# Kernel tuning notes

Hardware: AMD Instinct MI355X
Metric: run time of the kernel (lower is better)

## Reference

```python
import jax, jax.numpy as jnp
import numpy as np

H = 16          # num_attention_heads
D = 64          # attention_head_size
BUCKET = 128    # bucket_size
MAX_BUCKETS = 32
TEMP = 0.75
SINKHORN_ITERS = 5
NOISE_KEY = 42  # fixed key for gumbel routing noise (deterministic reference)


def _sinkhorn_route(pl, W, key):
    # pl: [b,h,buckets,d] bucket summaries, W: [h,d,buckets]
    R = jnp.einsum('bhid,hdf->bhif', pl, W)  # [b,h,buckets,buckets]
    u = jax.random.uniform(key, R.shape, R.dtype)
    gumbel = -jnp.log(-jnp.log(u + 1e-6) + 1e-6)
    R = (R + gumbel) / TEMP
    for _ in range(SINKHORN_ITERS):
        R = R - jax.scipy.special.logsumexp(R, axis=-1, keepdims=True)
        R = R - jax.scipy.special.logsumexp(R, axis=-2, keepdims=True)
    return jnp.exp(R)


def setup_inputs() -> dict:
    key = jax.random.key(0)
    kq, kk, kv, kwk, kwv = jax.random.split(key, 5)
    q = jax.random.normal(kq, (64, 4096, 64), jnp.float32)
    k = jax.random.normal(kk, (64, 4096, 64), jnp.float32)
    v = jax.random.normal(kv, (64, 4096, 64), jnp.float32)
    W_keys = jax.random.normal(kwk, (H, D, MAX_BUCKETS), jnp.float32)
    W_vals = jax.random.normal(kwv, (H, D, MAX_BUCKETS), jnp.float32)
    return {'q': q, 'k': k, 'v': v, 'W_keys': W_keys, 'W_vals': W_vals}


def reference(q, q_unused=None, *, _=None, **__):
    raise RuntimeError  # placeholder, replaced below


def reference(q, k, v, W_keys, W_vals):
    t, d = q.shape[1], q.shape[2]
    buckets = t // BUCKET
    # [b, h, buckets, bucket_size, d]
    b_q = q.reshape(-1, H, buckets, BUCKET, d)
    b_k = k.reshape(-1, H, buckets, BUCKET, d)
    b_v = v.reshape(-1, H, buckets, BUCKET, d)

    pl_k = b_k.sum(axis=-2)  # [b,h,buckets,d]
    R_k = _sinkhorn_route(pl_k, W_keys[..., :buckets], jax.random.key(NOISE_KEY))
    # NOTE: original also computes R_v / b_v_r but never uses them for output.

    b_k = jnp.einsum('bhij,bhjsd->bhisd', R_k, b_k) + b_k

    dots = jnp.einsum('bhuid,bhujd->bhuij', b_q, b_k) * (d ** -0.5)
    probs = jax.nn.softmax(dots, axis=-1)
    out = jnp.einsum('bhuij,bhujd->bhuid', probs, b_v)  # [b,h,buckets,s,d]
    return out.reshape(-1, t, d)
```

## Files before the change

### kernel.cpp

```cpp
#include <hip/hip_runtime.h>
#include <math.h>

#define BH 64
#define NB 32
#define BS 128
#define DHEAD 64

typedef __attribute__((ext_vector_type(8))) short bf16x8;
typedef __attribute__((ext_vector_type(4))) float f32x4;

#define LDVT 128
#define LDP 136


__device__ __forceinline__ unsigned rotl32(unsigned x, int d) {
    return (x << d) | (x >> (32 - d));
}

__device__ __forceinline__ void threefry2x32(unsigned k0, unsigned k1,
                                             unsigned& x0, unsigned& x1) {
    const unsigned ks0 = k0, ks1 = k1, ks2 = k0 ^ k1 ^ 0x1BD11BDAu;
    const int r0[4] = {13, 15, 26, 6};
    const int r1[4] = {17, 29, 16, 24};
    x0 += ks0; x1 += ks1;
    #pragma unroll
    for (int i = 0; i < 4; i++) { x0 += x1; x1 = rotl32(x1, r0[i]); x1 ^= x0; }
    x0 += ks1; x1 += ks2 + 1u;
    #pragma unroll
    for (int i = 0; i < 4; i++) { x0 += x1; x1 = rotl32(x1, r1[i]); x1 ^= x0; }
    x0 += ks2; x1 += ks0 + 2u;
    #pragma unroll
    for (int i = 0; i < 4; i++) { x0 += x1; x1 = rotl32(x1, r0[i]); x1 ^= x0; }
    x0 += ks0; x1 += ks1 + 3u;
    #pragma unroll
    for (int i = 0; i < 4; i++) { x0 += x1; x1 = rotl32(x1, r1[i]); x1 ^= x0; }
    x0 += ks1; x1 += ks2 + 4u;
    #pragma unroll
    for (int i = 0; i < 4; i++) { x0 += x1; x1 = rotl32(x1, r0[i]); x1 ^= x0; }
    x0 += ks2; x1 += ks0 + 5u;
}

__device__ __forceinline__ float jax_uniform_part(unsigned f) {
    unsigned x0 = 0u, x1 = f;
    threefry2x32(0u, 42u, x0, x1);
    unsigned bits = x0 ^ x1;
    return __uint_as_float((bits >> 9) | 0x3F800000u) - 1.0f;
}

__global__ void __launch_bounds__(256)
pl_kernel(const float* __restrict__ k, float* __restrict__ pl) {
    int blk = blockIdx.x;
    int tid = threadIdx.x;
    int w = tid >> 6, l = tid & 63;
    int rcls = l >> 4, c4 = l & 15;
    const float4* base = (const float4*)(k + (size_t)blk * 8192);

    float4 acc = {0.f, 0.f, 0.f, 0.f};
    #pragma unroll
    for (int t = 0; t < 8; t++) {
        float4 x = base[(w * 32 + t * 4 + rcls) * 16 + c4];
        acc.x += x.x; acc.y += x.y; acc.z += x.z; acc.w += x.w;
    }
    #pragma unroll
    for (int off = 16; off < 64; off <<= 1) {
        acc.x += __shfl_xor(acc.x, off);
        acc.y += __shfl_xor(acc.y, off);
        acc.z += __shfl_xor(acc.z, off);
        acc.w += __shfl_xor(acc.w, off);
    }
    __shared__ float4 red[4][16];
    if (rcls == 0) red[w][c4] = acc;
    __syncthreads();
    if (tid < 64) {
        int g = tid >> 2, j = tid & 3;
        float s = ((const float*)&red[0][g])[j] + ((const float*)&red[1][g])[j]
                + ((const float*)&red[2][g])[j] + ((const float*)&red[3][g])[j];
        pl[blk * 64 + tid] = s;
    }
}

__global__ void route_kernel(const float* __restrict__ pl, const float* __restrict__ Wk,
                             float* __restrict__ Rout) {
    int bh = blockIdx.x;
    int h = bh & 15;
    int tid = threadIdx.x;
    int i = tid >> 5, j = tid & 31;

    __shared__ float plS[NB * DHEAD];
    __shared__ float T[32 * 33];
    __shared__ float colL[32];

    for (int x = tid; x < NB * DHEAD; x += 1024) plS[x] = pl[bh * NB * DHEAD + x];
    __syncthreads();

    float acc = 0.f;
    #pragma unroll 8
    for (int d2 = 0; d2 < DHEAD; d2++)
        acc += plS[i * DHEAD + d2] * Wk[(h * DHEAD + d2) * NB + j];

    unsigned f = (unsigned)bh * 1024u + (unsigned)i * 32u + (unsigned)j;
    float u = jax_uniform_part(f);
    float g = -__logf(-__logf(u + 1e-6f) + 1e-6f);
    float val = (acc + g) / 0.75f;

    for (int it = 0; it < 5; it++) {
        float m = val;
        #pragma unroll
        for (int off = 1; off < 32; off <<= 1) m = fmaxf(m, __shfl_xor(m, off, 32));
        float s = __expf(val - m);
        #pragma unroll
        for (int off = 1; off < 32; off <<= 1) s += __shfl_xor(s, off, 32);
        val -= m + __logf(s);

        T[i * 33 + j] = val;
        __syncthreads();
        float tv = T[j * 33 + i];
        float m2 = tv;
        #pragma unroll
        for (int off = 1; off < 32; off <<= 1) m2 = fmaxf(m2, __shfl_xor(m2, off, 32));
        float s2 = __expf(tv - m2);
        #pragma unroll
        for (int off = 1; off < 32; off <<= 1) s2 += __shfl_xor(s2, off, 32);
        if (j == 0) colL[i] = m2 + __logf(s2);
        __syncthreads();
        val -= colL[j];
    }
    Rout[bh * 1024 + i * 32 + j] = __expf(val) + (i == j ? 1.0f : 0.0f);
}

__global__ void __launch_bounds__(256)
mix_kernel(const float* __restrict__ k, const float* __restrict__ Rp,
           unsigned short* __restrict__ khl) {
    __shared__ float X[32][260];
    int bh = blockIdx.x >> 5;
    int tile = blockIdx.x & 31;
    const size_t kbase = (size_t)bh * 262144;
    const int col0 = tile * 256;

    {
        int j = threadIdx.x >> 3;
        int cs = (threadIdx.x & 7) * 32;
        const float4* src = (const float4*)(k + kbase + (size_t)j * 8192 + col0 + cs);
        #pragma unroll
        for (int t = 0; t < 8; t++)
            *((float4*)&X[j][cs + 4 * t]) = src[t];
    }
    __syncthreads();

    const int col = threadIdx.x;
    float xv[32];
    #pragma unroll
    for (int j = 0; j < 32; j++) xv[j] = X[j][col];

    const float* Rb = Rp + bh * 1024;
    const int slot = col0 + col;
    const int s = slot >> 6, d = slot & 63;
    const int idx = s * 64 + (d ^ ((s & 7) << 3));
    const bool even = (col & 1) == 0;

    #pragma unroll 4
    for (int i = 0; i < 32; i++) {
        float acc = 0.f;
        #pragma unroll
        for (int j = 0; j < 32; j++) acc = fmaf(Rb[i * 32 + j], xv[j], acc);
        unsigned kb = __float_as_uint(acc);
        unsigned hiu = kb >> 16;
        float rem = acc - __uint_as_float(kb & 0xFFFF0000u);
        unsigned lou = __float_as_uint(rem) >> 16;
        unsigned oh = (unsigned)__shfl_xor((int)hiu, 1);
        unsigned ol = (unsigned)__shfl_xor((int)lou, 1);
        if (even) {
            unsigned short* bp = khl + ((size_t)(bh * 32 + i) << 14);
            *(unsigned*)&bp[idx]        = hiu | (oh << 16);
            *(unsigned*)&bp[idx + 8192] = lou | (ol << 16);
        }
    }
}

__global__ void __launch_bounds__(256)
attn_mfma_kernel(const float* __restrict__ q, const unsigned short* __restrict__ khl,
                 const float* __restrict__ v, float* __restrict__ out) {
    __shared__ __align__(16) unsigned short smem[8192 + 17408];
    unsigned short* VtS = smem;
    unsigned short* KhS = smem + 8192;
    unsigned short* KlS = smem + 16384;
    unsigned short* PbS = smem + 8192;

    const int tid = threadIdx.x;
    const int w = tid >> 6, lane = tid & 63;
    const int quad = lane >> 4, l15 = lane & 15;
    const int row0 = 32 * w;
    const size_t base = (size_t)blockIdx.x * (BS * DHEAD);

    {
        const char* src = (const char*)(khl + ((size_t)blockIdx.x << 14)) + tid * 16;
        char* dst = (char*)KhS + tid * 16;
        #pragma unroll
        for (int c = 0; c < 8; c++)
            __builtin_amdgcn_global_load_lds(
                (const __attribute__((address_space(1))) unsigned int*)(src + c * 4096),
                (__attribute__((address_space(3))) unsigned int*)(dst + c * 4096),
                16, 0, 0);
    }

    {
        int rp = tid >> 2;
        int c0 = (tid & 3) * 16;
        const float* v0 = v + base + (size_t)(2 * rp) * DHEAD + c0;
        const float* v1 = v0 + DHEAD;
        #pragma unroll
        for (int x = 0; x < 4; x++) {
            float4 a = ((const float4*)v0)[x];
            float4 b = ((const float4*)v1)[x];
            float fa[4] = {a.x, a.y, a.z, a.w};
            float fb[4] = {b.x, b.y, b.z, b.w};
            #pragma unroll
            for (int y = 0; y < 4; y++) {
                int c = c0 + 4 * x + y;
                unsigned lo = (__float_as_uint(fa[y]) + 0x8000u) >> 16;
                unsigned hi = (__float_as_uint(fb[y]) + 0x8000u) >> 16;
                unsigned swz = ((unsigned)((c ^ (c >> 4)) & 15)) << 3;
                unsigned idx = (unsigned)c * LDVT + (((unsigned)(2 * rp)) ^ swz);
                *(unsigned*)&VtS[idx] = lo | (hi << 16);
            }
        }
    }

    bf16x8 qh[2][2], ql[2][2];
    #pragma unroll
    for (int ti = 0; ti < 2; ti++) {
        #pragma unroll
        for (int kk = 0; kk < 2; kk++) {
            const float* qp = q + base + (size_t)(row0 + 16 * ti + l15) * DHEAD
                              + kk * 32 + quad * 8;
            float4 a = ((const float4*)qp)[0];
            float4 b = ((const float4*)qp)[1];
            float f[8] = {a.x, a.y, a.z, a.w, b.x, b.y, b.z, b.w};
            #pragma unroll
            for (int j = 0; j < 8; j++) {
                float qs = f[j] * 0.125f;
                unsigned bits = __float_as_uint(qs);
                unsigned short hi = (unsigned short)(bits >> 16);
                float rem = qs - __uint_as_float(bits & 0xFFFF0000u);
                unsigned short lo = (unsigned short)(__float_as_uint(rem) >> 16);
                qh[ti][kk][j] = (short)hi;
                ql[ti][kk][j] = (short)lo;
            }
        }
    }
    __syncthreads();

    f32x4 acc[2][8];
    #pragma unroll
    for (int ti = 0; ti < 2; ti++)
        #pragma unroll
        for (int tc = 0; tc < 8; tc++)
            acc[ti][tc] = (f32x4){0.f, 0.f, 0.f, 0.f};

    #pragma unroll
    for (int tc = 0; tc < 8; tc++) {
        const int jrow = 16 * tc + l15;
        const int swzk = (jrow & 7) << 3;
        const int rbase = jrow * 64;
        bf16x8 bh0 = *(const bf16x8*)&KhS[rbase + ((quad * 8 + 0)  ^ swzk)];
        bf16x8 bh1 = *(const bf16x8*)&KhS[rbase + ((quad * 8 + 32) ^ swzk)];
        bf16x8 bl0 = *(const bf16x8*)&KlS[rbase + ((quad * 8 + 0)  ^ swzk)];
        bf16x8 bl1 = *(const bf16x8*)&KlS[rbase + ((quad * 8 + 32) ^ swzk)];
        __builtin_amdgcn_s_setprio(1);
        #pragma unroll
        for (int ti = 0; ti < 2; ti++) {
            f32x4 c = acc[ti][tc];
            c = __builtin_amdgcn_mfma_f32_16x16x32_bf16(qh[ti][0], bh0, c, 0, 0, 0);
            c = __builtin_amdgcn_mfma_f32_16x16x32_bf16(qh[ti][1], bh1, c, 0, 0, 0);
            c = __builtin_amdgcn_mfma_f32_16x16x32_bf16(ql[ti][0], bh0, c, 0, 0, 0);
            c = __builtin_amdgcn_mfma_f32_16x16x32_bf16(ql[ti][1], bh1, c, 0, 0, 0);
            c = __builtin_amdgcn_mfma_f32_16x16x32_bf16(qh[ti][0], bl0, c, 0, 0, 0);
            c = __builtin_amdgcn_mfma_f32_16x16x32_bf16(qh[ti][1], bl1, c, 0, 0, 0);
            acc[ti][tc] = c;
        }
        __builtin_amdgcn_s_setprio(0);
    }

    float mrow[2][4], lrow[2][4];
    #pragma unroll
    for (int ti = 0; ti < 2; ti++)
        #pragma unroll
        for (int r = 0; r < 4; r++) {
            float m = acc[ti][0][r];
            #pragma unroll
            for (int tc = 1; tc < 8; tc++) m = fmaxf(m, acc[ti][tc][r]);
            #pragma unroll
            for (int off = 1; off < 16; off <<= 1)
                m = fmaxf(m, __shfl_xor(m, off, 64));
            mrow[ti][r] = m;
        }
    #pragma unroll
    for (int ti = 0; ti < 2; ti++)
        #pragma unroll
        for (int r = 0; r < 4; r++) {
            float s = 0.f;
            #pragma unroll
            for (int tc = 0; tc < 8; tc++) {
                float p = __expf(acc[ti][tc][r] - mrow[ti][r]);
                acc[ti][tc][r] = p;
                s += p;
            }
            #pragma unroll
            for (int off = 1; off < 16; off <<= 1)
                s += __shfl_xor(s, off, 64);
            lrow[ti][r] = s;
        }

    __syncthreads();

    #pragma unroll
    for (int ti = 0; ti < 2; ti++)
        #pragma unroll
        for (int tc = 0; tc < 8; tc++)
            #pragma unroll
            for (int r = 0; r < 4; r++) {
                int prow = row0 + 16 * ti + quad * 4 + r;
                unsigned pb = __float_as_uint(acc[ti][tc][r]);
                PbS[prow * LDP + 16 * tc + l15] = (unsigned short)((pb + 0x8000u) >> 16);
            }
    __syncthreads();

    f32x4 oacc[2][4];
    #pragma unroll
    for (int ti = 0; ti < 2; ti++)
        #pragma unroll
        for (int tc = 0; tc < 4; tc++)
            oacc[ti][tc] = (f32x4){0.f, 0.f, 0.f, 0.f};

    #pragma unroll
    for (int kc = 0; kc < 4; kc++) {
        bf16x8 aP[2];
        #pragma unroll
        for (int ti = 0; ti < 2; ti++)
            aP[ti] = *(const bf16x8*)&PbS[(row0 + 16 * ti + l15) * LDP + kc * 32 + quad * 8];
        __builtin_amdgcn_s_setprio(1);
        #pragma unroll
        for (int tc = 0; tc < 4; tc++) {
            unsigned n = (unsigned)(16 * tc + l15);
            unsigned swz = ((n ^ (n >> 4)) & 15u) << 3;
            unsigned idx = n * LDVT + (((unsigned)(kc * 32 + quad * 8)) ^ swz);
            bf16x8 vb = *(const bf16x8*)&VtS[idx];
            #pragma unroll
            for (int ti = 0; ti < 2; ti++)
                oacc[ti][tc] = __builtin_amdgcn_mfma_f32_16x16x32_bf16(aP[ti], vb, oacc[ti][tc], 0, 0, 0);
        }
        __builtin_amdgcn_s_setprio(0);
    }

    float inv[2][4];
    #pragma unroll
    for (int ti = 0; ti < 2; ti++)
        #pragma unroll
        for (int r = 0; r < 4; r++) inv[ti][r] = 1.0f / lrow[ti][r];

    #pragma unroll
    for (int ti = 0; ti < 2; ti++)
        #pragma unroll
        for (int tc = 0; tc < 4; tc++)
            #pragma unroll
            for (int r = 0; r < 4; r++) {
                int orow = row0 + 16 * ti + quad * 4 + r;
                out[base + (size_t)orow * DHEAD + 16 * tc + l15] = oacc[ti][tc][r] * inv[ti][r];
            }
}

extern "C" void kernel_launch(void* const* d_in, const int* in_sizes, int n_in,
                              void* d_out, int out_size, void* d_ws, size_t ws_size,
                              hipStream_t stream) {
    const float* q  = (const float*)d_in[0];
    const float* k  = (const float*)d_in[1];
    const float* v  = (const float*)d_in[2];
    const float* Wk = (const float*)d_in[3];
    float* out = (float*)d_out;

    unsigned short* khl = (unsigned short*)d_ws;
    float* pl = (float*)(khl + (size_t)33554432);
    float* R  = pl + (size_t)131072;

    pl_kernel<<<dim3(BH * NB), dim3(256), 0, stream>>>(k, pl);
    route_kernel<<<dim3(BH), dim3(1024), 0, stream>>>(pl, Wk, R);
    mix_kernel<<<dim3(BH * NB), dim3(256), 0, stream>>>(k, R, khl);
    attn_mfma_kernel<<<dim3(BH * NB), dim3(256), 0, stream>>>(q, khl, v, out);
}
```

Before: 276.3 us.

## Keep softmax probabilities in registers via bpermute and shrink LDS footprint

The QK^T MFMA operands are swapped so each lane holds a full query row's scores, which allows row max/sum reductions with just two cross-quad shuffles. Probabilities are normalized and packed to bf16 in registers, then redistributed into the PV A-operand layout with ds_bpermute instead of a round trip through a padded LDS buffer. V is held in registers until K is consumed so V^T can reuse K's LDS space, cutting shared memory from about 50KB to 32KB, and launch bounds ask for 4 blocks per SM. This trades extra register pressure and permute instructions for higher occupancy and less LDS traffic.

```diff
diff --git a/kernel.cpp b/kernel.cpp
--- a/kernel.cpp
+++ b/kernel.cpp
@@ -10,7 +10,6 @@
 typedef __attribute__((ext_vector_type(4))) float f32x4;
 
 #define LDVT 128
-#define LDP 136
 
 
 __device__ __forceinline__ unsigned rotl32(unsigned x, int d) {
@@ -45,6 +44,10 @@
     threefry2x32(0u, 42u, x0, x1);
     unsigned bits = x0 ^ x1;
     return __uint_as_float((bits >> 9) | 0x3F800000u) - 1.0f;
+}
+
+__device__ __forceinline__ unsigned rn16(float x) {
+    return (__float_as_uint(x) + 0x8000u) >> 16;
 }
 
 __global__ void __launch_bounds__(256)
@@ -177,14 +180,13 @@
     }
 }
 
-__global__ void __launch_bounds__(256)
+__global__ void __launch_bounds__(256, 4)
 attn_mfma_kernel(const float* __restrict__ q, const unsigned short* __restrict__ khl,
                  const float* __restrict__ v, float* __restrict__ out) {
-    __shared__ __align__(16) unsigned short smem[8192 + 17408];
+    __shared__ __align__(16) unsigned short smem[16384];
+    unsigned short* KhS = smem;
+    unsigned short* KlS = smem + 8192;
     unsigned short* VtS = smem;
-    unsigned short* KhS = smem + 8192;
-    unsigned short* KlS = smem + 16384;
-    unsigned short* PbS = smem + 8192;
 
     const int tid = threadIdx.x;
     const int w = tid >> 6, lane = tid & 63;
@@ -203,10 +205,11 @@
                 16, 0, 0);
     }
 
+    const int rp = tid >> 2;
+    const int c0v = (tid & 3) * 16;
+    unsigned vt[16];
     {
-        int rp = tid >> 2;
-        int c0 = (tid & 3) * 16;
-        const float* v0 = v + base + (size_t)(2 * rp) * DHEAD + c0;
+        const float* v0 = v + base + (size_t)(2 * rp) * DHEAD + c0v;
         const float* v1 = v0 + DHEAD;
         #pragma unroll
         for (int x = 0; x < 4; x++) {
@@ -215,14 +218,8 @@
             float fa[4] = {a.x, a.y, a.z, a.w};
             float fb[4] = {b.x, b.y, b.z, b.w};
             #pragma unroll
-            for (int y = 0; y < 4; y++) {
-                int c = c0 + 4 * x + y;
-                unsigned lo = (__float_as_uint(fa[y]) + 0x8000u) >> 16;
-                unsigned hi = (__float_as_uint(fb[y]) + 0x8000u) >> 16;
-                unsigned swz = ((unsigned)((c ^ (c >> 4)) & 15)) << 3;
-                unsigned idx = (unsigned)c * LDVT + (((unsigned)(2 * rp)) ^ swz);
-                *(unsigned*)&VtS[idx] = lo | (hi << 16);
-            }
+            for (int y = 0; y < 4; y++)
+                vt[4 * x + y] = rn16(fa[y]) | (rn16(fb[y]) << 16);
         }
     }
 
@@ -262,67 +259,68 @@
         const int jrow = 16 * tc + l15;
         const int swzk = (jrow & 7) << 3;
         const int rbase = jrow * 64;
-        bf16x8 bh0 = *(const bf16x8*)&KhS[rbase + ((quad * 8 + 0)  ^ swzk)];
-        bf16x8 bh1 = *(const bf16x8*)&KhS[rbase + ((quad * 8 + 32) ^ swzk)];
-        bf16x8 bl0 = *(const bf16x8*)&KlS[rbase + ((quad * 8 + 0)  ^ swzk)];
-        bf16x8 bl1 = *(const bf16x8*)&KlS[rbase + ((quad * 8 + 32) ^ swzk)];
+        bf16x8 kh0 = *(const bf16x8*)&KhS[rbase + ((quad * 8 + 0)  ^ swzk)];
+        bf16x8 kh1 = *(const bf16x8*)&KhS[rbase + ((quad * 8 + 32) ^ swzk)];
+        bf16x8 kl0 = *(const bf16x8*)&KlS[rbase + ((quad * 8 + 0)  ^ swzk)];
+        bf16x8 kl1 = *(const bf16x8*)&KlS[rbase + ((quad * 8 + 32) ^ swzk)];
         __builtin_amdgcn_s_setprio(1);
         #pragma unroll
         for (int ti = 0; ti < 2; ti++) {
             f32x4 c = acc[ti][tc];
-            c = __builtin_amdgcn_mfma_f32_16x16x32_bf16(qh[ti][0], bh0, c, 0, 0, 0);
-            c = __builtin_amdgcn_mfma_f32_16x16x32_bf16(qh[ti][1], bh1, c, 0, 0, 0);
-            c = __builtin_amdgcn_mfma_f32_16x16x32_bf16(ql[ti][0], bh0, c, 0, 0, 0);
-            c = __builtin_amdgcn_mfma_f32_16x16x32_bf16(ql[ti][1], bh1, c, 0, 0, 0);
-            c = __builtin_amdgcn_mfma_f32_16x16x32_bf16(qh[ti][0], bl0, c, 0, 0, 0);
-            c = __builtin_amdgcn_mfma_f32_16x16x32_bf16(qh[ti][1], bl1, c, 0, 0, 0);
+            c = __builtin_amdgcn_mfma_f32_16x16x32_bf16(kh0, qh[ti][0], c, 0, 0, 0);
+            c = __builtin_amdgcn_mfma_f32_16x16x32_bf16(kh1, qh[ti][1], c, 0, 0, 0);
+            c = __builtin_amdgcn_mfma_f32_16x16x32_bf16(kh0, ql[ti][0], c, 0, 0, 0);
+            c = __builtin_amdgcn_mfma_f32_16x16x32_bf16(kh1, ql[ti][1], c, 0, 0, 0);
+            c = __builtin_amdgcn_mfma_f32_16x16x32_bf16(kl0, qh[ti][0], c, 0, 0, 0);
+            c = __builtin_amdgcn_mfma_f32_16x16x32_bf16(kl1, qh[ti][1], c, 0, 0, 0);
             acc[ti][tc] = c;
         }
         __builtin_amdgcn_s_setprio(0);
     }
 
-    float mrow[2][4], lrow[2][4];
-    #pragma unroll
-    for (int ti = 0; ti < 2; ti++)
-        #pragma unroll
-        for (int r = 0; r < 4; r++) {
-            float m = acc[ti][0][r];
-            #pragma unroll
-            for (int tc = 1; tc < 8; tc++) m = fmaxf(m, acc[ti][tc][r]);
-            #pragma unroll
-            for (int off = 1; off < 16; off <<= 1)
-                m = fmaxf(m, __shfl_xor(m, off, 64));
-            mrow[ti][r] = m;
-        }
-    #pragma unroll
-    for (int ti = 0; ti < 2; ti++)
-        #pragma unroll
-        for (int r = 0; r < 4; r++) {
-            float s = 0.f;
-            #pragma unroll
-            for (int tc = 0; tc < 8; tc++) {
-                float p = __expf(acc[ti][tc][r] - mrow[ti][r]);
+    unsigned pkA[2][8], pkB[2][8];
+    #pragma unroll
+    for (int ti = 0; ti < 2; ti++) {
+        float m = acc[ti][0][0];
+        #pragma unroll
+        for (int tc = 0; tc < 8; tc++)
+            #pragma unroll
+            for (int r = 0; r < 4; r++)
+                m = fmaxf(m, acc[ti][tc][r]);
+        m = fmaxf(m, __shfl_xor(m, 16));
+        m = fmaxf(m, __shfl_xor(m, 32));
+        float s = 0.f;
+        #pragma unroll
+        for (int tc = 0; tc < 8; tc++)
+            #pragma unroll
+            for (int r = 0; r < 4; r++) {
+                float p = __expf(acc[ti][tc][r] - m);
                 acc[ti][tc][r] = p;
                 s += p;
             }
-            #pragma unroll
-            for (int off = 1; off < 16; off <<= 1)
-                s += __shfl_xor(s, off, 64);
-            lrow[ti][r] = s;
-        }
-
-    __syncthreads();
-
-    #pragma unroll
-    for (int ti = 0; ti < 2; ti++)
-        #pragma unroll
-        for (int tc = 0; tc < 8; tc++)
-            #pragma unroll
-            for (int r = 0; r < 4; r++) {
-                int prow = row0 + 16 * ti + quad * 4 + r;
-                unsigned pb = __float_as_uint(acc[ti][tc][r]);
-                PbS[prow * LDP + 16 * tc + l15] = (unsigned short)((pb + 0x8000u) >> 16);
+        s += __shfl_xor(s, 16);
+        s += __shfl_xor(s, 32);
+        float inv = 1.0f / s;
+        #pragma unroll
+        for (int tc = 0; tc < 8; tc++) {
+            pkA[ti][tc] = rn16(acc[ti][tc][0] * inv) | (rn16(acc[ti][tc][1] * inv) << 16);
+            pkB[ti][tc] = rn16(acc[ti][tc][2] * inv) | (rn16(acc[ti][tc][3] * inv) << 16);
+        }
+    }
+
+    __syncthreads();
+
+    {
+        #pragma unroll
+        for (int x = 0; x < 4; x++)
+            #pragma unroll
+            for (int y = 0; y < 4; y++) {
+                int c = c0v + 4 * x + y;
+                unsigned swz = ((unsigned)((c ^ (c >> 4)) & 15)) << 3;
+                unsigned idx = (unsigned)c * LDVT + (((unsigned)(2 * rp)) ^ swz);
+                *(unsigned*)&VtS[idx] = vt[4 * x + y];
             }
+    }
     __syncthreads();
 
     f32x4 oacc[2][4];
@@ -332,12 +330,30 @@
         for (int tc = 0; tc < 4; tc++)
             oacc[ti][tc] = (f32x4){0.f, 0.f, 0.f, 0.f};
 
+    const int a0 = ((((2 * quad) & 3) * 16 + l15) << 2);
+    const int a1 = ((((2 * quad + 1) & 3) * 16 + l15) << 2);
+    const bool hiTile = (quad >> 1) != 0;
+
     #pragma unroll
     for (int kc = 0; kc < 4; kc++) {
-        bf16x8 aP[2];
-        #pragma unroll
-        for (int ti = 0; ti < 2; ti++)
-            aP[ti] = *(const bf16x8*)&PbS[(row0 + 16 * ti + l15) * LDP + kc * 32 + quad * 8];
+        bf16x8 pa[2];
+        #pragma unroll
+        for (int ti = 0; ti < 2; ti++) {
+            unsigned uA0 = (unsigned)__builtin_amdgcn_ds_bpermute(a0, (int)pkA[ti][2 * kc]);
+            unsigned uA1 = (unsigned)__builtin_amdgcn_ds_bpermute(a0, (int)pkA[ti][2 * kc + 1]);
+            unsigned uB0 = (unsigned)__builtin_amdgcn_ds_bpermute(a0, (int)pkB[ti][2 * kc]);
+            unsigned uB1 = (unsigned)__builtin_amdgcn_ds_bpermute(a0, (int)pkB[ti][2 * kc + 1]);
+            unsigned vA0 = (unsigned)__builtin_amdgcn_ds_bpermute(a1, (int)pkA[ti][2 * kc]);
+            unsigned vA1 = (unsigned)__builtin_amdgcn_ds_bpermute(a1, (int)pkA[ti][2 * kc + 1]);
+            unsigned vB0 = (unsigned)__builtin_amdgcn_ds_bpermute(a1, (int)pkB[ti][2 * kc]);
+            unsigned vB1 = (unsigned)__builtin_amdgcn_ds_bpermute(a1, (int)pkB[ti][2 * kc + 1]);
+            union { unsigned u[4]; bf16x8 v; } pu;
+            pu.u[0] = hiTile ? uA1 : uA0;
+            pu.u[1] = hiTile ? uB1 : uB0;
+            pu.u[2] = hiTile ? vA1 : vA0;
+            pu.u[3] = hiTile ? vB1 : vB0;
+            pa[ti] = pu.v;
+        }
         __builtin_amdgcn_s_setprio(1);
         #pragma unroll
         for (int tc = 0; tc < 4; tc++) {
@@ -347,16 +363,10 @@
             bf16x8 vb = *(const bf16x8*)&VtS[idx];
             #pragma unroll
             for (int ti = 0; ti < 2; ti++)
-                oacc[ti][tc] = __builtin_amdgcn_mfma_f32_16x16x32_bf16(aP[ti], vb, oacc[ti][tc], 0, 0, 0);
+                oacc[ti][tc] = __builtin_amdgcn_mfma_f32_16x16x32_bf16(pa[ti], vb, oacc[ti][tc], 0, 0, 0);
         }
         __builtin_amdgcn_s_setprio(0);
     }
-
-    float inv[2][4];
-    #pragma unroll
-    for (int ti = 0; ti < 2; ti++)
-        #pragma unroll
-        for (int r = 0; r < 4; r++) inv[ti][r] = 1.0f / lrow[ti][r];
 
     #pragma unroll
     for (int ti = 0; ti < 2; ti++)
@@ -365,7 +375,7 @@
             #pragma unroll
             for (int r = 0; r < 4; r++) {
                 int orow = row0 + 16 * ti + quad * 4 + r;
-                out[base + (size_t)orow * DHEAD + 16 * tc + l15] = oacc[ti][tc][r] * inv[ti][r];
+                out[base + (size_t)orow * DHEAD + 16 * tc + l15] = oacc[ti][tc][r];
             }
 }
 
```

Result: no change. 280.2 us (+1.4%).
